# Kernel optimization log

Measured on AMD Instinct MI355X. Metric: run time of the kernel, lower is better.

## Reference

```python
import jax, jax.numpy as jnp
import numpy as np

D_MODEL = 1024
H = 16
D_K = D_MODEL // H
B = 2
S = 2048
NEG = -1e10


def setup_inputs() -> dict:
    key = jax.random.key(0)
    ks = jax.random.split(key, 12)
    sc = 1.0 / np.sqrt(D_MODEL)
    inp = {
        "q": jax.random.normal(ks[0], (B, S, D_MODEL), jnp.float32),
        "k": jax.random.normal(ks[1], (B, S, D_MODEL), jnp.float32),
        "v": jax.random.normal(ks[2], (B, S, D_MODEL), jnp.float32),
        # causal mask, broadcast over batch and heads
        "mask": jnp.tril(jnp.ones((S, S), jnp.int32))[None, None, :, :],
        "w_q": jax.random.normal(ks[3], (D_MODEL, D_MODEL), jnp.float32) * sc,
        "b_q": jax.random.normal(ks[4], (D_MODEL,), jnp.float32) * sc,
        "w_k": jax.random.normal(ks[5], (D_MODEL, D_MODEL), jnp.float32) * sc,
        "b_k": jax.random.normal(ks[6], (D_MODEL,), jnp.float32) * sc,
        "w_v": jax.random.normal(ks[7], (D_MODEL, D_MODEL), jnp.float32) * sc,
        "b_v": jax.random.normal(ks[8], (D_MODEL,), jnp.float32) * sc,
        "w_o": jax.random.normal(ks[9], (D_MODEL, D_MODEL), jnp.float32) * sc,
        "b_o": jax.random.normal(ks[10], (D_MODEL,), jnp.float32) * sc,
    }
    return inp


def _split_heads(x):
    # [B, S, D] -> [B, H, S, d_k]
    b, s, _ = x.shape
    return x.reshape(b, s, H, D_K).transpose(0, 2, 1, 3)


def reference(q, k, v, mask, w_q, b_q, w_k, b_k, w_v, b_v, w_o, b_o):
    # Linear projections (torch Linear: x @ W.T + b)
    qh = _split_heads(q @ w_q.T + b_q)
    kh = _split_heads(k @ w_k.T + b_k)
    vh = _split_heads(v @ w_v.T + b_v)
    scale = 1.0 / jnp.sqrt(jnp.asarray(D_K, qh.dtype))
    scores = jnp.einsum("bhqd,bhkd->bhqk", qh, kh) * scale
    scores = jnp.where(mask == 0, jnp.asarray(NEG, scores.dtype), scores)
    attn = jax.nn.softmax(scores, axis=-1)  # dropout=0.0 -> identity
    x = jnp.einsum("bhqk,bhkd->bhqd", attn, vh)
    x = x.transpose(0, 2, 1, 3).reshape(q.shape[0], -1, H * D_K)
    out = x @ w_o.T + b_o
    return (out, attn)
```

## Files before the change

### kernel.cpp

```cpp
#include <hip/hip_runtime.h>
#include <hip/hip_bf16.h>

typedef unsigned short u16;
typedef unsigned int u32;
typedef __attribute__((ext_vector_type(8))) short bf16x8;
typedef __attribute__((ext_vector_type(4))) float f32x4;

#define SEQ 2048
#define DM 1024
#define NH 16
#define DKK 64
#define NB 2

__device__ __forceinline__ u16 f2bf(float f) {
  union { float f; u32 u; } x; x.f = f;
  u32 r = x.u + 0x7FFFu + ((x.u >> 16) & 1u);
  return (u16)(r >> 16);
}

__device__ __forceinline__ void gl_lds16(const void* g, void* l) {
  __builtin_amdgcn_global_load_lds(
      (const __attribute__((address_space(1))) u32*)g,
      (__attribute__((address_space(3))) u32*)l, 16, 0, 0);
}

#define MFMA16(a, b, c) __builtin_amdgcn_mfma_f32_16x16x32_bf16(a, b, c, 0, 0, 0)
#define VMCNT0() asm volatile("s_waitcnt vmcnt(0)" ::: "memory")
#define SCHEDB() __builtin_amdgcn_sched_barrier(0)

struct CvtArgs {
  const float* in[7];
  u16* out[7];
  int n4[7];
};

__global__ __launch_bounds__(256) void cvt_all(CvtArgs a) {
  const int y = blockIdx.y;
  const float* in = a.in[y];
  u16* out = a.out[y];
  const int n4 = a.n4[y];
  int i = blockIdx.x * 256 + threadIdx.x;
  if (i >= n4) return;
  float4 v = ((const float4*)in)[i];
  ushort4 o;
  o.x = f2bf(v.x); o.y = f2bf(v.y); o.z = f2bf(v.z); o.w = f2bf(v.w);
  ((ushort4*)out)[i] = o;
}

struct ProjArgs {
  const u16* A;
  const u16* W;
  const float* bias;
  u16* Y;
  float scale;
};

__global__ __launch_bounds__(256) void proj_qkv(ProjArgs a0, ProjArgs a1,
                                                ProjArgs a2) {
  ProjArgs pa = (blockIdx.z == 0) ? a0 : (blockIdx.z == 1) ? a1 : a2;
  __shared__ __align__(16) u16 As[2][128 * 32];
  __shared__ __align__(16) u16 Bs[2][128 * 32];
  const int tid = threadIdx.x, lane = tid & 63, w = tid >> 6;
  const int lr = lane & 15, lg = lane >> 4;
  const int wr = w >> 1, wc = w & 1;
  const int r0 = blockIdx.x * 128, c0 = blockIdx.y * 128;
  f32x4 acc[4][4];
#pragma unroll
  for (int i = 0; i < 4; ++i)
#pragma unroll
    for (int j = 0; j < 4; ++j) acc[i][j] = (f32x4){0.f, 0.f, 0.f, 0.f};

  auto stage = [&](int k0, int buf) {
#pragma unroll
    for (int c = 0; c < 2; ++c) {
      int idx = tid + 256 * c;
      int row = idx >> 2, seg = idx & 3;
      gl_lds16(pa.A + (size_t)(r0 + row) * DM + k0 + seg * 8,
               (char*)As[buf] + idx * 16);
      gl_lds16(pa.W + (size_t)(c0 + row) * DM + k0 + seg * 8,
               (char*)Bs[buf] + idx * 16);
    }
  };

  stage(0, 0);
  __syncthreads();
  int buf = 0;
  const int NT = DM / 32;
  for (int t = 0; t < NT; ++t) {
    if (t + 1 < NT) stage((t + 1) * 32, buf ^ 1);
    bf16x8 a[4], b[4];
#pragma unroll
    for (int i = 0; i < 4; ++i) {
      int row = wr * 64 + i * 16 + lr;
      a[i] = *(const bf16x8*)((const char*)As[buf] + row * 64 + lg * 16);
    }
#pragma unroll
    for (int j = 0; j < 4; ++j) {
      int row = wc * 64 + j * 16 + lr;
      b[j] = *(const bf16x8*)((const char*)Bs[buf] + row * 64 + lg * 16);
    }
#pragma unroll
    for (int i = 0; i < 4; ++i)
#pragma unroll
      for (int j = 0; j < 4; ++j) acc[i][j] = MFMA16(a[i], b[j], acc[i][j]);
    __syncthreads();
    buf ^= 1;
  }
#pragma unroll
  for (int i = 0; i < 4; ++i)
#pragma unroll
    for (int j = 0; j < 4; ++j)
#pragma unroll
      for (int rg = 0; rg < 4; ++rg) {
        int row = r0 + wr * 64 + i * 16 + lg * 4 + rg;
        int col = c0 + wc * 64 + j * 16 + lr;
        float v = (acc[i][j][rg] + pa.bias[col]) * pa.scale;
        int bb = row >> 11, s = row & (SEQ - 1), h = col >> 6, d = col & 63;
        pa.Y[((size_t)(bb * NH + h) * SEQ + s) * DKK + d] = f2bf(v);
      }
}

__global__ __launch_bounds__(256) void mm_out(const u16* __restrict__ A,
                                              const u16* __restrict__ W,
                                              const float* __restrict__ bias,
                                              float* __restrict__ Y) {
  __shared__ __align__(16) u16 As[2][128 * 32];
  __shared__ __align__(16) u16 Bs[2][128 * 32];
  const int tid = threadIdx.x, lane = tid & 63, w = tid >> 6;
  const int lr = lane & 15, lg = lane >> 4;
  const int wr = w >> 1, wc = w & 1;
  const int r0 = blockIdx.x * 128, c0 = blockIdx.y * 128;
  f32x4 acc[4][4];
#pragma unroll
  for (int i = 0; i < 4; ++i)
#pragma unroll
    for (int j = 0; j < 4; ++j) acc[i][j] = (f32x4){0.f, 0.f, 0.f, 0.f};

  auto stage = [&](int k0, int buf) {
#pragma unroll
    for (int c = 0; c < 2; ++c) {
      int idx = tid + 256 * c;
      int row = idx >> 2, seg = idx & 3;
      gl_lds16(A + (size_t)(r0 + row) * DM + k0 + seg * 8,
               (char*)As[buf] + idx * 16);
      gl_lds16(W + (size_t)(c0 + row) * DM + k0 + seg * 8,
               (char*)Bs[buf] + idx * 16);
    }
  };

  stage(0, 0);
  __syncthreads();
  int buf = 0;
  const int NT = DM / 32;
  for (int t = 0; t < NT; ++t) {
    if (t + 1 < NT) stage((t + 1) * 32, buf ^ 1);
    bf16x8 a[4], b[4];
#pragma unroll
    for (int i = 0; i < 4; ++i) {
      int row = wr * 64 + i * 16 + lr;
      a[i] = *(const bf16x8*)((const char*)As[buf] + row * 64 + lg * 16);
    }
#pragma unroll
    for (int j = 0; j < 4; ++j) {
      int row = wc * 64 + j * 16 + lr;
      b[j] = *(const bf16x8*)((const char*)Bs[buf] + row * 64 + lg * 16);
    }
#pragma unroll
    for (int i = 0; i < 4; ++i)
#pragma unroll
      for (int j = 0; j < 4; ++j) acc[i][j] = MFMA16(a[i], b[j], acc[i][j]);
    __syncthreads();
    buf ^= 1;
  }
#pragma unroll
  for (int i = 0; i < 4; ++i)
#pragma unroll
    for (int j = 0; j < 4; ++j)
#pragma unroll
      for (int rg = 0; rg < 4; ++rg) {
        int row = r0 + wr * 64 + i * 16 + lg * 4 + rg;
        int col = c0 + wc * 64 + j * 16 + lr;
        Y[(size_t)row * DM + col] = acc[i][j][rg] + bias[col];
      }
}

__global__ __launch_bounds__(256) void transpose_v(const u16* __restrict__ Vh,
                                                   u16* __restrict__ Vt) {
  const int st = blockIdx.x, bh = blockIdx.y;
  const u16* src = Vh + ((size_t)bh * SEQ + st * 64) * DKK;
  u16* dst = Vt + (size_t)bh * DKK * SEQ + st * 64;
  __shared__ u16 T[64][68];
  const int tid = threadIdx.x;
#pragma unroll
  for (int c = 0; c < 4; ++c) {
    int idx = tid + 256 * c;
    int r = idx >> 4, seg = idx & 15;
    ushort4 v = *(const ushort4*)(src + r * 64 + seg * 4);
    *(ushort4*)&T[r][seg * 4] = v;
  }
  __syncthreads();
#pragma unroll
  for (int c = 0; c < 4; ++c) {
    int idx = tid + 256 * c;
    int d = idx >> 4, sseg = idx & 15;
    ushort4 o;
    o.x = T[sseg * 4 + 0][d]; o.y = T[sseg * 4 + 1][d];
    o.z = T[sseg * 4 + 2][d]; o.w = T[sseg * 4 + 3][d];
    *(ushort4*)(dst + (size_t)d * SEQ + sseg * 4) = o;
  }
}

__global__ __launch_bounds__(256) void flash_attn(const u16* __restrict__ Qh,
                                                  const u16* __restrict__ Kh,
                                                  const u16* __restrict__ Vt,
                                                  u16* __restrict__ X,
                                                  float* __restrict__ attn) {
  const int lin = (int)(blockIdx.y * gridDim.x + blockIdx.x);
  const int nwg = (int)(gridDim.x * gridDim.y);
  const int swz = (lin & 7) * (nwg >> 3) + (lin >> 3);
  const int qi = (int)gridDim.x - 1 - (swz & 15);
  const int bh = swz >> 4;
  const int q0 = qi * 128;
  const u16* Qb = Qh + (size_t)bh * SEQ * DKK;
  const u16* Kb = Kh + (size_t)bh * SEQ * DKK;
  const u16* Vb = Vt + (size_t)bh * DKK * SEQ;
  float* attb = attn + (size_t)bh * SEQ * SEQ;
  const int tid = threadIdx.x, lane = tid & 63, w = tid >> 6;
  const int lr = lane & 15, lg = lane >> 4;

  __shared__ __align__(16) u16 Ks[2][64 * 64];
  __shared__ __align__(16) u16 Vs[2][64 * 64];
  __shared__ __align__(16) u16 Ps[4 * 32 * 64];

  bf16x8 frQ[2][2];
#pragma unroll
  for (int ri = 0; ri < 2; ++ri)
#pragma unroll
    for (int kc = 0; kc < 2; ++kc) {
      int r = q0 + w * 32 + ri * 16 + lr;
      frQ[ri][kc] = *(const bf16x8*)(Qb + (size_t)r * DKK + kc * 32 + lg * 8);
    }

  const int wmax = q0 + w * 32 + 31;
  const int nkv = (qi + 1) * 2;

  auto stageK = [&](int j, int buf) {
    const int kv0 = j * 64;
#pragma unroll
    for (int c = 0; c < 2; ++c) {
      int idx = tid + 256 * c;
      int row = idx >> 3, sq = idx & 7;
      int seg = sq ^ (row & 7);
      gl_lds16(Kb + (size_t)(kv0 + row) * DKK + seg * 8,
               (char*)Ks[buf] + idx * 16);
    }
  };
  auto stageV = [&](int j, int buf) {
    const int kv0 = j * 64;
#pragma unroll
    for (int c = 0; c < 2; ++c) {
      int idx = tid + 256 * c;
      int row = idx >> 3, sq = idx & 7;
      int seg = sq ^ (row & 7);
      gl_lds16(Vb + (size_t)row * SEQ + kv0 + seg * 8,
               (char*)Vs[buf] + idx * 16);
    }
  };

  float rs[2] = {0.f, 0.f};
  stageK(0, 0);
  VMCNT0();
  __builtin_amdgcn_s_barrier();
  SCHEDB();
  for (int j = 0; j < nkv; ++j) {
    const int buf = j & 1;
    const int kv0 = j * 64;
    if (j + 1 < nkv) stageK(j + 1, buf ^ 1);
    if (kv0 <= wmax) {
      __builtin_amdgcn_s_setprio(1);
#pragma unroll
      for (int ci = 0; ci < 4; ++ci) {
        bf16x8 aK[2];
#pragma unroll
        for (int kc = 0; kc < 2; ++kc) {
          int row = ci * 16 + lr;
          int q = (kc * 4 + lg) ^ (row & 7);
          aK[kc] = *(const bf16x8*)((const char*)Ks[buf] + row * 128 + q * 16);
        }
#pragma unroll
        for (int ri = 0; ri < 2; ++ri) {
          f32x4 a = (f32x4){0.f, 0.f, 0.f, 0.f};
          a = MFMA16(aK[0], frQ[ri][0], a);
          a = MFMA16(aK[1], frQ[ri][1], a);
          const int qglob = q0 + w * 32 + ri * 16 + lr;
#pragma unroll
          for (int rg = 0; rg < 4; ++rg) {
            int kvglob = kv0 + ci * 16 + lg * 4 + rg;
            rs[ri] += (kvglob <= qglob) ? __expf(a[rg]) : 0.f;
          }
        }
      }
      __builtin_amdgcn_s_setprio(0);
    }
    VMCNT0();
    __builtin_amdgcn_s_barrier();
    SCHEDB();
  }
  float vinv[2];
#pragma unroll
  for (int ri = 0; ri < 2; ++ri) {
    float v = rs[ri];
    v += __shfl_xor(v, 16);
    v += __shfl_xor(v, 32);
    vinv[ri] = 1.f / v;
  }

  f32x4 accO[2][4];
#pragma unroll
  for (int ri = 0; ri < 2; ++ri)
#pragma unroll
    for (int ci = 0; ci < 4; ++ci) accO[ri][ci] = (f32x4){0.f, 0.f, 0.f, 0.f};

  stageK(0, 0);
  stageV(0, 0);
  VMCNT0();
  __builtin_amdgcn_s_barrier();
  SCHEDB();
  for (int j = 0; j < nkv; ++j) {
    const int buf = j & 1;
    const int kv0 = j * 64;
    if (j + 1 < nkv) {
      stageK(j + 1, buf ^ 1);
      stageV(j + 1, buf ^ 1);
    }
    if (kv0 <= wmax) {
      __builtin_amdgcn_s_setprio(1);
      f32x4 sf[4][2];
#pragma unroll
      for (int ci = 0; ci < 4; ++ci) {
        bf16x8 aK[2];
#pragma unroll
        for (int kc = 0; kc < 2; ++kc) {
          int row = ci * 16 + lr;
          int q = (kc * 4 + lg) ^ (row & 7);
          aK[kc] = *(const bf16x8*)((const char*)Ks[buf] + row * 128 + q * 16);
        }
#pragma unroll
        for (int ri = 0; ri < 2; ++ri) {
          f32x4 a = (f32x4){0.f, 0.f, 0.f, 0.f};
          a = MFMA16(aK[0], frQ[ri][0], a);
          a = MFMA16(aK[1], frQ[ri][1], a);
          sf[ci][ri] = a;
        }
      }
#pragma unroll
      for (int ri = 0; ri < 2; ++ri) {
        const int qglob = q0 + w * 32 + ri * 16 + lr;
        const int qlrow = ri * 16 + lr;
        float* orow = attb + (size_t)qglob * SEQ;
#pragma unroll
        for (int ci = 0; ci < 4; ++ci) {
          float p[4];
#pragma unroll
          for (int rg = 0; rg < 4; ++rg) {
            int kvglob = kv0 + ci * 16 + lg * 4 + rg;
            p[rg] = (kvglob <= qglob) ? __expf(sf[ci][ri][rg]) * vinv[ri] : 0.f;
          }
          float4 o = {p[0], p[1], p[2], p[3]};
          *(float4*)(orow + kv0 + ci * 16 + lg * 4) = o;
          u32 lo = (u32)f2bf(p[0]) | ((u32)f2bf(p[1]) << 16);
          u32 hi = (u32)f2bf(p[2]) | ((u32)f2bf(p[3]) << 16);
          int c16 = (ci * 2 + (lg >> 1)) ^ (lr & 7);
          char* dst = (char*)Ps + w * 4096 + qlrow * 128 + c16 * 16 +
                      (lg & 1) * 8;
          *(uint2*)dst = (uint2){lo, hi};
        }
      }
#pragma unroll
      for (int kvc = 0; kvc < 2; ++kvc) {
        bf16x8 aP[2];
#pragma unroll
        for (int ri = 0; ri < 2; ++ri) {
          int qlrow = ri * 16 + lr;
          int c16 = (kvc * 4 + lg) ^ (lr & 7);
          aP[ri] = *(const bf16x8*)((const char*)Ps + w * 4096 + qlrow * 128 +
                                    c16 * 16);
        }
#pragma unroll
        for (int ci = 0; ci < 4; ++ci) {
          int row = ci * 16 + lr;
          int q2 = (kvc * 4 + lg) ^ (row & 7);
          bf16x8 bV =
              *(const bf16x8*)((const char*)Vs[buf] + row * 128 + q2 * 16);
#pragma unroll
          for (int ri = 0; ri < 2; ++ri)
            accO[ri][ci] = MFMA16(aP[ri], bV, accO[ri][ci]);
        }
      }
      __builtin_amdgcn_s_setprio(0);
    } else {
      const float4 z = {0.f, 0.f, 0.f, 0.f};
#pragma unroll
      for (int ri = 0; ri < 2; ++ri) {
        const int qglob = q0 + w * 32 + ri * 16 + lr;
        float* orow = attb + (size_t)qglob * SEQ;
#pragma unroll
        for (int ci = 0; ci < 4; ++ci)
          *(float4*)(orow + kv0 + ci * 16 + lg * 4) = z;
      }
    }
    VMCNT0();
    __builtin_amdgcn_s_barrier();
    SCHEDB();
  }

  {
    const float4 z = {0.f, 0.f, 0.f, 0.f};
    for (int j = nkv; j < SEQ / 64; ++j) {
      const int kv0 = j * 64;
#pragma unroll
      for (int ri = 0; ri < 2; ++ri) {
        const int qglob = q0 + w * 32 + ri * 16 + lr;
        float* orow = attb + (size_t)qglob * SEQ;
#pragma unroll
        for (int ci = 0; ci < 4; ++ci)
          *(float4*)(orow + kv0 + ci * 16 + lg * 4) = z;
      }
    }
  }

  const int b = bh >> 4, h = bh & (NH - 1);
#pragma unroll
  for (int ri = 0; ri < 2; ++ri)
#pragma unroll
    for (int ci = 0; ci < 4; ++ci)
#pragma unroll
      for (int rg = 0; rg < 4; ++rg) {
        int srow = q0 + w * 32 + ri * 16 + lg * 4 + rg;
        int col = h * DKK + ci * 16 + lr;
        X[((size_t)(b * SEQ + srow)) * DM + col] = f2bf(accO[ri][ci][rg]);
      }
}

extern "C" void kernel_launch(void* const* d_in, const int* in_sizes, int n_in,
                              void* d_out, int out_size, void* d_ws,
                              size_t ws_size, hipStream_t stream) {
  const float* q = (const float*)d_in[0];
  const float* k = (const float*)d_in[1];
  const float* v = (const float*)d_in[2];
  const float* w_q = (const float*)d_in[4];
  const float* b_q = (const float*)d_in[5];
  const float* w_k = (const float*)d_in[6];
  const float* b_k = (const float*)d_in[7];
  const float* w_v = (const float*)d_in[8];
  const float* b_v = (const float*)d_in[9];
  const float* w_o = (const float*)d_in[10];
  const float* b_o = (const float*)d_in[11];

  float* out = (float*)d_out;
  float* attn = out + (size_t)NB * SEQ * DM;

  const size_t MB = 1u << 20;
  char* ws = (char*)d_ws;
  u16* qb = (u16*)(ws);
  u16* kb = (u16*)(ws + 8 * MB);
  u16* vb = (u16*)(ws + 16 * MB);
  u16* Qh = (u16*)(ws + 24 * MB);
  u16* Kh = (u16*)(ws + 32 * MB);
  u16* Vh = (u16*)(ws + 40 * MB);
  u16* wqb = (u16*)(ws + 48 * MB);
  u16* wkb = (u16*)(ws + 50 * MB);
  u16* wvb = (u16*)(ws + 52 * MB);
  u16* wob = (u16*)(ws + 54 * MB);
  u16* Vt = qb;
  u16* X = vb;

  dim3 blk(256);
  const int n4_qkv = NB * SEQ * DM / 4;
  const int n4_w = DM * DM / 4;

  CvtArgs ca;
  ca.in[0] = q;   ca.out[0] = qb;  ca.n4[0] = n4_qkv;
  ca.in[1] = k;   ca.out[1] = kb;  ca.n4[1] = n4_qkv;
  ca.in[2] = v;   ca.out[2] = vb;  ca.n4[2] = n4_qkv;
  ca.in[3] = w_q; ca.out[3] = wqb; ca.n4[3] = n4_w;
  ca.in[4] = w_k; ca.out[4] = wkb; ca.n4[4] = n4_w;
  ca.in[5] = w_v; ca.out[5] = wvb; ca.n4[5] = n4_w;
  ca.in[6] = w_o; ca.out[6] = wob; ca.n4[6] = n4_w;
  cvt_all<<<dim3((n4_qkv + 255) / 256, 7), blk, 0, stream>>>(ca);

  ProjArgs aq = {qb, wqb, b_q, Qh, 0.125f};
  ProjArgs ak = {kb, wkb, b_k, Kh, 1.0f};
  ProjArgs av = {vb, wvb, b_v, Vh, 1.0f};
  proj_qkv<<<dim3(NB * SEQ / 128, DM / 128, 3), blk, 0, stream>>>(aq, ak, av);

  transpose_v<<<dim3(SEQ / 64, NB * NH), blk, 0, stream>>>(Vh, Vt);

  flash_attn<<<dim3(SEQ / 128, NB * NH), blk, 0, stream>>>(Qh, Kh, Vt, X,
                                                           attn);

  mm_out<<<dim3(NB * SEQ / 128, DM / 128), blk, 0, stream>>>(X, wob, b_o, out);
}
```

Before: 290.0 us.

## Shrink attention query tile, use nontemporal attn stores, relax waitcnt, swap GEMM grid order

```diff
diff --git a/kernel.cpp b/kernel.cpp
--- a/kernel.cpp
+++ b/kernel.cpp
@@ -24,8 +24,13 @@
       (__attribute__((address_space(3))) u32*)l, 16, 0, 0);
 }
 
+__device__ __forceinline__ void nt_store4(float* p, f32x4 v) {
+  __builtin_nontemporal_store(v, (f32x4*)p);
+}
+
 #define MFMA16(a, b, c) __builtin_amdgcn_mfma_f32_16x16x32_bf16(a, b, c, 0, 0, 0)
 #define VMCNT0() asm volatile("s_waitcnt vmcnt(0)" ::: "memory")
+#define VMCNT4() asm volatile("s_waitcnt vmcnt(4)" ::: "memory")
 #define SCHEDB() __builtin_amdgcn_sched_barrier(0)
 
 struct CvtArgs {
@@ -63,7 +68,7 @@
   const int tid = threadIdx.x, lane = tid & 63, w = tid >> 6;
   const int lr = lane & 15, lg = lane >> 4;
   const int wr = w >> 1, wc = w & 1;
-  const int r0 = blockIdx.x * 128, c0 = blockIdx.y * 128;
+  const int c0 = blockIdx.x * 128, r0 = blockIdx.y * 128;
   f32x4 acc[4][4];
 #pragma unroll
   for (int i = 0; i < 4; ++i)
@@ -129,7 +134,7 @@
   const int tid = threadIdx.x, lane = tid & 63, w = tid >> 6;
   const int lr = lane & 15, lg = lane >> 4;
   const int wr = w >> 1, wc = w & 1;
-  const int r0 = blockIdx.x * 128, c0 = blockIdx.y * 128;
+  const int c0 = blockIdx.x * 128, r0 = blockIdx.y * 128;
   f32x4 acc[4][4];
 #pragma unroll
   for (int i = 0; i < 4; ++i)
@@ -216,11 +221,10 @@
                                                   u16* __restrict__ X,
                                                   float* __restrict__ attn) {
   const int lin = (int)(blockIdx.y * gridDim.x + blockIdx.x);
-  const int nwg = (int)(gridDim.x * gridDim.y);
-  const int swz = (lin & 7) * (nwg >> 3) + (lin >> 3);
-  const int qi = (int)gridDim.x - 1 - (swz & 15);
-  const int bh = swz >> 4;
-  const int q0 = qi * 128;
+  const int swz = (lin & 7) * 128 + (lin >> 3);
+  const int qi = 31 - (swz & 31);
+  const int bh = swz >> 5;
+  const int q0 = qi * 64;
   const u16* Qb = Qh + (size_t)bh * SEQ * DKK;
   const u16* Kb = Kh + (size_t)bh * SEQ * DKK;
   const u16* Vb = Vt + (size_t)bh * DKK * SEQ;
@@ -230,19 +234,18 @@
 
   __shared__ __align__(16) u16 Ks[2][64 * 64];
   __shared__ __align__(16) u16 Vs[2][64 * 64];
-  __shared__ __align__(16) u16 Ps[4 * 32 * 64];
-
-  bf16x8 frQ[2][2];
-#pragma unroll
-  for (int ri = 0; ri < 2; ++ri)
-#pragma unroll
-    for (int kc = 0; kc < 2; ++kc) {
-      int r = q0 + w * 32 + ri * 16 + lr;
-      frQ[ri][kc] = *(const bf16x8*)(Qb + (size_t)r * DKK + kc * 32 + lg * 8);
-    }
-
-  const int wmax = q0 + w * 32 + 31;
-  const int nkv = (qi + 1) * 2;
+  __shared__ __align__(16) u16 Ps[4 * 16 * 64];
+
+  bf16x8 frQ[2];
+#pragma unroll
+  for (int kc = 0; kc < 2; ++kc) {
+    int r = q0 + w * 16 + lr;
+    frQ[kc] = *(const bf16x8*)(Qb + (size_t)r * DKK + kc * 32 + lg * 8);
+  }
+
+  const int qglob = q0 + w * 16 + lr;
+  const int wmax = q0 + w * 16 + 15;
+  const int nkv = qi + 1;
 
   auto stageK = [&](int j, int buf) {
     const int kv0 = j * 64;
@@ -267,7 +270,7 @@
     }
   };
 
-  float rs[2] = {0.f, 0.f};
+  float rs = 0.f;
   stageK(0, 0);
   VMCNT0();
   __builtin_amdgcn_s_barrier();
@@ -287,17 +290,13 @@
           int q = (kc * 4 + lg) ^ (row & 7);
           aK[kc] = *(const bf16x8*)((const char*)Ks[buf] + row * 128 + q * 16);
         }
-#pragma unroll
-        for (int ri = 0; ri < 2; ++ri) {
-          f32x4 a = (f32x4){0.f, 0.f, 0.f, 0.f};
-          a = MFMA16(aK[0], frQ[ri][0], a);
-          a = MFMA16(aK[1], frQ[ri][1], a);
-          const int qglob = q0 + w * 32 + ri * 16 + lr;
-#pragma unroll
-          for (int rg = 0; rg < 4; ++rg) {
-            int kvglob = kv0 + ci * 16 + lg * 4 + rg;
-            rs[ri] += (kvglob <= qglob) ? __expf(a[rg]) : 0.f;
-          }
+        f32x4 a = (f32x4){0.f, 0.f, 0.f, 0.f};
+        a = MFMA16(aK[0], frQ[0], a);
+        a = MFMA16(aK[1], frQ[1], a);
+#pragma unroll
+        for (int rg = 0; rg < 4; ++rg) {
+          int kvglob = kv0 + ci * 16 + lg * 4 + rg;
+          rs += (kvglob <= qglob) ? __expf(a[rg]) : 0.f;
         }
       }
       __builtin_amdgcn_s_setprio(0);
@@ -306,20 +305,13 @@
     __builtin_amdgcn_s_barrier();
     SCHEDB();
   }
-  float vinv[2];
-#pragma unroll
-  for (int ri = 0; ri < 2; ++ri) {
-    float v = rs[ri];
-    v += __shfl_xor(v, 16);
-    v += __shfl_xor(v, 32);
-    vinv[ri] = 1.f / v;
-  }
-
-  f32x4 accO[2][4];
-#pragma unroll
-  for (int ri = 0; ri < 2; ++ri)
-#pragma unroll
-    for (int ci = 0; ci < 4; ++ci) accO[ri][ci] = (f32x4){0.f, 0.f, 0.f, 0.f};
+  rs += __shfl_xor(rs, 16);
+  rs += __shfl_xor(rs, 32);
+  const float vinv = 1.f / rs;
+
+  f32x4 accO[4];
+#pragma unroll
+  for (int ci = 0; ci < 4; ++ci) accO[ci] = (f32x4){0.f, 0.f, 0.f, 0.f};
 
   stageK(0, 0);
   stageV(0, 0);
@@ -335,7 +327,7 @@
     }
     if (kv0 <= wmax) {
       __builtin_amdgcn_s_setprio(1);
-      f32x4 sf[4][2];
+      f32x4 sf[4];
 #pragma unroll
       for (int ci = 0; ci < 4; ++ci) {
         bf16x8 aK[2];
@@ -345,101 +337,75 @@
           int q = (kc * 4 + lg) ^ (row & 7);
           aK[kc] = *(const bf16x8*)((const char*)Ks[buf] + row * 128 + q * 16);
         }
-#pragma unroll
-        for (int ri = 0; ri < 2; ++ri) {
-          f32x4 a = (f32x4){0.f, 0.f, 0.f, 0.f};
-          a = MFMA16(aK[0], frQ[ri][0], a);
-          a = MFMA16(aK[1], frQ[ri][1], a);
-          sf[ci][ri] = a;
+        f32x4 a = (f32x4){0.f, 0.f, 0.f, 0.f};
+        a = MFMA16(aK[0], frQ[0], a);
+        a = MFMA16(aK[1], frQ[1], a);
+        sf[ci] = a;
+      }
+      float* orow = attb + (size_t)qglob * SEQ;
+#pragma unroll
+      for (int ci = 0; ci < 4; ++ci) {
+        float p[4];
+#pragma unroll
+        for (int rg = 0; rg < 4; ++rg) {
+          int kvglob = kv0 + ci * 16 + lg * 4 + rg;
+          p[rg] = (kvglob <= qglob) ? __expf(sf[ci][rg]) * vinv : 0.f;
         }
-      }
-#pragma unroll
-      for (int ri = 0; ri < 2; ++ri) {
-        const int qglob = q0 + w * 32 + ri * 16 + lr;
-        const int qlrow = ri * 16 + lr;
-        float* orow = attb + (size_t)qglob * SEQ;
-#pragma unroll
-        for (int ci = 0; ci < 4; ++ci) {
-          float p[4];
-#pragma unroll
-          for (int rg = 0; rg < 4; ++rg) {
-            int kvglob = kv0 + ci * 16 + lg * 4 + rg;
-            p[rg] = (kvglob <= qglob) ? __expf(sf[ci][ri][rg]) * vinv[ri] : 0.f;
-          }
-          float4 o = {p[0], p[1], p[2], p[3]};
-          *(float4*)(orow + kv0 + ci * 16 + lg * 4) = o;
-          u32 lo = (u32)f2bf(p[0]) | ((u32)f2bf(p[1]) << 16);
-          u32 hi = (u32)f2bf(p[2]) | ((u32)f2bf(p[3]) << 16);
-          int c16 = (ci * 2 + (lg >> 1)) ^ (lr & 7);
-          char* dst = (char*)Ps + w * 4096 + qlrow * 128 + c16 * 16 +
-                      (lg & 1) * 8;
-          *(uint2*)dst = (uint2){lo, hi};
-        }
+        f32x4 o = {p[0], p[1], p[2], p[3]};
+        nt_store4(orow + kv0 + ci * 16 + lg * 4, o);
+        u32 lo = (u32)f2bf(p[0]) | ((u32)f2bf(p[1]) << 16);
+        u32 hi = (u32)f2bf(p[2]) | ((u32)f2bf(p[3]) << 16);
+        int c16 = (ci * 2 + (lg >> 1)) ^ (lr & 7);
+        char* dst = (char*)Ps + w * 2048 + lr * 128 + c16 * 16 + (lg & 1) * 8;
+        *(uint2*)dst = (uint2){lo, hi};
       }
 #pragma unroll
       for (int kvc = 0; kvc < 2; ++kvc) {
-        bf16x8 aP[2];
-#pragma unroll
-        for (int ri = 0; ri < 2; ++ri) {
-          int qlrow = ri * 16 + lr;
-          int c16 = (kvc * 4 + lg) ^ (lr & 7);
-          aP[ri] = *(const bf16x8*)((const char*)Ps + w * 4096 + qlrow * 128 +
-                                    c16 * 16);
-        }
+        int c16a = (kvc * 4 + lg) ^ (lr & 7);
+        bf16x8 aP =
+            *(const bf16x8*)((const char*)Ps + w * 2048 + lr * 128 + c16a * 16);
 #pragma unroll
         for (int ci = 0; ci < 4; ++ci) {
           int row = ci * 16 + lr;
           int q2 = (kvc * 4 + lg) ^ (row & 7);
           bf16x8 bV =
               *(const bf16x8*)((const char*)Vs[buf] + row * 128 + q2 * 16);
-#pragma unroll
-          for (int ri = 0; ri < 2; ++ri)
-            accO[ri][ci] = MFMA16(aP[ri], bV, accO[ri][ci]);
+          accO[ci] = MFMA16(aP, bV, accO[ci]);
         }
       }
       __builtin_amdgcn_s_setprio(0);
     } else {
-      const float4 z = {0.f, 0.f, 0.f, 0.f};
-#pragma unroll
-      for (int ri = 0; ri < 2; ++ri) {
-        const int qglob = q0 + w * 32 + ri * 16 + lr;
-        float* orow = attb + (size_t)qglob * SEQ;
-#pragma unroll
-        for (int ci = 0; ci < 4; ++ci)
-          *(float4*)(orow + kv0 + ci * 16 + lg * 4) = z;
-      }
-    }
-    VMCNT0();
+      const f32x4 z = {0.f, 0.f, 0.f, 0.f};
+      float* orow = attb + (size_t)qglob * SEQ;
+#pragma unroll
+      for (int ci = 0; ci < 4; ++ci)
+        nt_store4(orow + kv0 + ci * 16 + lg * 4, z);
+    }
+    VMCNT4();
     __builtin_amdgcn_s_barrier();
     SCHEDB();
   }
 
   {
-    const float4 z = {0.f, 0.f, 0.f, 0.f};
+    const f32x4 z = {0.f, 0.f, 0.f, 0.f};
+    float* orow = attb + (size_t)qglob * SEQ;
     for (int j = nkv; j < SEQ / 64; ++j) {
       const int kv0 = j * 64;
 #pragma unroll
-      for (int ri = 0; ri < 2; ++ri) {
-        const int qglob = q0 + w * 32 + ri * 16 + lr;
-        float* orow = attb + (size_t)qglob * SEQ;
-#pragma unroll
-        for (int ci = 0; ci < 4; ++ci)
-          *(float4*)(orow + kv0 + ci * 16 + lg * 4) = z;
-      }
+      for (int ci = 0; ci < 4; ++ci)
+        nt_store4(orow + kv0 + ci * 16 + lg * 4, z);
     }
   }
 
   const int b = bh >> 4, h = bh & (NH - 1);
 #pragma unroll
-  for (int ri = 0; ri < 2; ++ri)
-#pragma unroll
-    for (int ci = 0; ci < 4; ++ci)
-#pragma unroll
-      for (int rg = 0; rg < 4; ++rg) {
-        int srow = q0 + w * 32 + ri * 16 + lg * 4 + rg;
-        int col = h * DKK + ci * 16 + lr;
-        X[((size_t)(b * SEQ + srow)) * DM + col] = f2bf(accO[ri][ci][rg]);
-      }
+  for (int ci = 0; ci < 4; ++ci)
+#pragma unroll
+    for (int rg = 0; rg < 4; ++rg) {
+      int srow = q0 + w * 16 + lg * 4 + rg;
+      int col = h * DKK + ci * 16 + lr;
+      X[((size_t)(b * SEQ + srow)) * DM + col] = f2bf(accO[ci][rg]);
+    }
 }
 
 extern "C" void kernel_launch(void* const* d_in, const int* in_sizes, int n_in,
@@ -492,12 +458,11 @@
   ProjArgs aq = {qb, wqb, b_q, Qh, 0.125f};
   ProjArgs ak = {kb, wkb, b_k, Kh, 1.0f};
   ProjArgs av = {vb, wvb, b_v, Vh, 1.0f};
-  proj_qkv<<<dim3(NB * SEQ / 128, DM / 128, 3), blk, 0, stream>>>(aq, ak, av);
+  proj_qkv<<<dim3(DM / 128, NB * SEQ / 128, 3), blk, 0, stream>>>(aq, ak, av);
 
   transpose_v<<<dim3(SEQ / 64, NB * NH), blk, 0, stream>>>(Vh, Vt);
 
-  flash_attn<<<dim3(SEQ / 128, NB * NH), blk, 0, stream>>>(Qh, Kh, Vt, X,
-                                                           attn);
-
-  mm_out<<<dim3(NB * SEQ / 128, DM / 128), blk, 0, stream>>>(X, wob, b_o, out);
-}
+  flash_attn<<<dim3(SEQ / 64, NB * NH), blk, 0, stream>>>(Qh, Kh, Vt, X, attn);
+
+  mm_out<<<dim3(DM / 128, NB * SEQ / 128), blk, 0, stream>>>(X, wob, b_o, out);
+}
```

New measurement: 325.9 us. +12.4%, slower.
